# Kernel optimization log

Hardware: AMD Instinct MI355X
Metric: run time of the kernel (lower is better)

The kernel has to match this reference:

```python
import jax, jax.numpy as jnp
import numpy as np

N_NODES = 100000
N_EDGES = 1600000
N_GRAPHS = 512
IN_C, HID_C, OUT_C = 128, 128, 64


def setup_inputs() -> dict:
    key = jax.random.key(0)
    ks = jax.random.split(key, 10)
    x = jax.random.normal(ks[0], (N_NODES, IN_C), dtype=jnp.float32)
    edge_index = jax.random.randint(ks[1], (2, N_EDGES), 0, N_NODES, dtype=jnp.int64)
    batch = jnp.sort(jax.random.randint(ks[2], (N_NODES,), 0, N_GRAPHS, dtype=jnp.int64))
    def glorot(k, shape):
        fan_in = shape[1]
        return jax.random.normal(k, shape, dtype=jnp.float32) / jnp.sqrt(jnp.float32(fan_in))
    return {
        "x": x, "edge_index": edge_index, "batch": batch,
        "w_nbr0": glorot(ks[3], (HID_C, IN_C)), "w_self0": glorot(ks[4], (HID_C, IN_C)), "b0": jnp.zeros((HID_C,), jnp.float32),
        "w_nbr1": glorot(ks[5], (HID_C, HID_C)), "w_self1": glorot(ks[6], (HID_C, HID_C)), "b1": jnp.zeros((HID_C,), jnp.float32),
        "w_nbr2": glorot(ks[7], (OUT_C, HID_C)), "w_self2": glorot(ks[8], (OUT_C, HID_C)), "b2": jnp.zeros((OUT_C,), jnp.float32),
    }


def _sage_conv(x, src, dst, w_nbr, w_self, b):
    n = x.shape[0]
    # mean aggregation of neighbor messages: gather x[src], segment-sum at dst
    agg = jax.ops.segment_sum(x[src], dst, num_segments=n)  # [N, d]
    deg = jax.ops.segment_sum(jnp.ones_like(dst, dtype=x.dtype), dst, num_segments=n)
    mean_nbr = agg / jnp.maximum(deg, 1.0)[:, None]
    return mean_nbr @ w_nbr.T + x @ w_self.T + b


def reference(x, edge_index, batch, w_nbr0, w_self0, b0, w_nbr1, w_self1, b1, w_nbr2, w_self2, b2):
    src, dst = edge_index[0], edge_index[1]
    h = jax.nn.relu(_sage_conv(x, src, dst, w_nbr0, w_self0, b0))
    h = jax.nn.relu(_sage_conv(h, src, dst, w_nbr1, w_self1, b1))
    h = _sage_conv(h, src, dst, w_nbr2, w_self2, b2)
    # global mean pool over graphs in the batch
    sums = jax.ops.segment_sum(h, batch, num_segments=N_GRAPHS)  # [G, out]
    cnts = jax.ops.segment_sum(jnp.ones_like(batch, dtype=h.dtype), batch, num_segments=N_GRAPHS)
    return sums / jnp.maximum(cnts, 1.0)[:, None]
```

## Files before the change

### kernel.cpp

```cpp
#include <hip/hip_runtime.h>
#include <hip/hip_bf16.h>

#define NGRAPHS 512
#define BCAP 8192

typedef __attribute__((ext_vector_type(8))) short bf16x8;
typedef __attribute__((ext_vector_type(4))) float f32x4;

__device__ inline short f2bf(float x) {
    __hip_bfloat16 h = __float2bfloat16(x);
    return *(short*)&h;
}
__device__ inline float bflo(uint v) { return __uint_as_float(v << 16); }
__device__ inline float bfhi(uint v) { return __uint_as_float(v & 0xffff0000u); }


__global__ __launch_bounds__(256) void k_bscatter(const int* __restrict__ src,
                                                  const int* __restrict__ dst,
                                                  int* __restrict__ bcur,
                                                  uint* __restrict__ pairs,
                                                  int nE, int NB) {
    __shared__ int cnt[512];
    __shared__ int gbase[512];
    const int t = threadIdx.x;
    const int seg0 = blockIdx.x * 4096;

    for (int l = t; l < NB; l += 256) cnt[l] = 0;
    __syncthreads();

    int sv[16], bv[16], rv[16];
#pragma unroll
    for (int k = 0; k < 16; ++k) {
        int e = seg0 + k * 256 + t;
        if (e < nE) {
            int d = dst[e];
            bv[k] = d >> 8;
            rv[k] = atomicAdd(&cnt[bv[k]], 1);
            sv[k] = src[e] | ((d & 255) << 20);
        } else {
            bv[k] = -1;
        }
    }
    __syncthreads();
    for (int l = t; l < NB; l += 256) {
        int c = cnt[l];
        gbase[l] = (c > 0) ? atomicAdd(&bcur[l], c) : 0;
    }
    __syncthreads();
#pragma unroll
    for (int k = 0; k < 16; ++k) {
        if (bv[k] >= 0) {
            int pos = gbase[bv[k]] + rv[k];
            if (pos < BCAP) pairs[(size_t)bv[k] * BCAP + pos] = (uint)sv[k];
        }
    }
}

__global__ __launch_bounds__(256) void k_bbuild(const int* __restrict__ bcur,
                                                const uint* __restrict__ pairs,
                                                int* __restrict__ row_start,
                                                int* __restrict__ row_end,
                                                float* __restrict__ rdeg,
                                                int* __restrict__ col, int n) {
    __shared__ int s[256];
    __shared__ int cur[256];
    const int b = blockIdx.x;
    const int t = threadIdx.x;
    const uint* bp = pairs + (size_t)b * BCAP;
    int cnt = bcur[b];
    if (cnt > BCAP) cnt = BCAP;

    s[t] = 0;
    __syncthreads();
    for (int i = t; i < cnt; i += 256) {
        int local = bp[i] >> 20;
        atomicAdd(&s[local], 1);
    }
    __syncthreads();
    int my = s[t];
    for (int off = 1; off < 256; off <<= 1) {
        int v = (t >= off) ? s[t - off] : 0;
        __syncthreads();
        s[t] += v;
        __syncthreads();
    }
    int excl = s[t] - my;
    int v = b * 256 + t;
    if (v < n) {
        row_start[v] = b * BCAP + excl;
        row_end[v] = b * BCAP + excl + my;
        rdeg[v] = 1.0f / (float)(my > 1 ? my : 1);
    }
    cur[t] = excl;
    __syncthreads();
    for (int i = t; i < cnt; i += 256) {
        uint u = bp[i];
        int local = u >> 20;
        int pos = atomicAdd(&cur[local], 1);
        col[(size_t)b * BCAP + pos] = (int)(u & 0xFFFFFu);
    }
}


__global__ __launch_bounds__(256) void k_cast(const float* __restrict__ x,
                                              ushort* __restrict__ xb, int total4) {
    int i = blockIdx.x * 256 + threadIdx.x;
    if (i >= total4) return;
    float4 v = ((const float4*)x)[i];
    ushort4 o;
    o.x = (ushort)f2bf(v.x);
    o.y = (ushort)f2bf(v.y);
    o.z = (ushort)f2bf(v.z);
    o.w = (ushort)f2bf(v.w);
    ((ushort4*)xb)[i] = o;
}


__global__ __launch_bounds__(256) void k_agg(const ushort* __restrict__ h,
                                             const int* __restrict__ row_start,
                                             const int* __restrict__ row_end,
                                             const int* __restrict__ col,
                                             const float* __restrict__ rdeg,
                                             ushort* __restrict__ out, int n) {
    int w = (blockIdx.x * blockDim.x + threadIdx.x) >> 6;
    int lane = threadIdx.x & 63;
    if (w >= n) return;
    int s = row_start[w], e = row_end[w];
    int grp = lane >> 4;
    int cl = lane & 15;

    float a0 = 0.f, a1 = 0.f, a2 = 0.f, a3 = 0.f, a4 = 0.f, a5 = 0.f, a6 = 0.f, a7 = 0.f;

    if (e > s) {
        int cfirst = col[s];
        for (int j = s; j < e; j += 8) {
            int j0 = j + grp, j1 = j + 4 + grp;
            bool ok0 = j0 < e, ok1 = j1 < e;
            int c0 = ok0 ? col[j0] : cfirst;
            int c1 = ok1 ? col[j1] : cfirst;
            uint4 r0 = *(const uint4*)(h + (size_t)c0 * 128 + cl * 8);
            uint4 r1 = *(const uint4*)(h + (size_t)c1 * 128 + cl * 8);
            if (ok0) {
                a0 += bflo(r0.x); a1 += bfhi(r0.x);
                a2 += bflo(r0.y); a3 += bfhi(r0.y);
                a4 += bflo(r0.z); a5 += bfhi(r0.z);
                a6 += bflo(r0.w); a7 += bfhi(r0.w);
            }
            if (ok1) {
                a0 += bflo(r1.x); a1 += bfhi(r1.x);
                a2 += bflo(r1.y); a3 += bfhi(r1.y);
                a4 += bflo(r1.z); a5 += bfhi(r1.z);
                a6 += bflo(r1.w); a7 += bfhi(r1.w);
            }
        }
        a0 += __shfl_xor(a0, 16); a1 += __shfl_xor(a1, 16);
        a2 += __shfl_xor(a2, 16); a3 += __shfl_xor(a3, 16);
        a4 += __shfl_xor(a4, 16); a5 += __shfl_xor(a5, 16);
        a6 += __shfl_xor(a6, 16); a7 += __shfl_xor(a7, 16);
        a0 += __shfl_xor(a0, 32); a1 += __shfl_xor(a1, 32);
        a2 += __shfl_xor(a2, 32); a3 += __shfl_xor(a3, 32);
        a4 += __shfl_xor(a4, 32); a5 += __shfl_xor(a5, 32);
        a6 += __shfl_xor(a6, 32); a7 += __shfl_xor(a7, 32);
    }

    if (grp == 0) {
        float r = rdeg[w];
        uint4 o;
        o.x = (uint)(ushort)f2bf(a0 * r) | ((uint)(ushort)f2bf(a1 * r) << 16);
        o.y = (uint)(ushort)f2bf(a2 * r) | ((uint)(ushort)f2bf(a3 * r) << 16);
        o.z = (uint)(ushort)f2bf(a4 * r) | ((uint)(ushort)f2bf(a5 * r) << 16);
        o.w = (uint)(ushort)f2bf(a6 * r) | ((uint)(ushort)f2bf(a7 * r) << 16);
        *(uint4*)(out + (size_t)w * 128 + cl * 8) = o;
    }
}


__global__ __launch_bounds__(256) void k_agg2(const ushort* __restrict__ t2,
                                              const int* __restrict__ row_start,
                                              const int* __restrict__ row_end,
                                              const int* __restrict__ col,
                                              const float* __restrict__ rdeg,
                                              ushort* __restrict__ out, int n) {
    int w = (blockIdx.x * blockDim.x + threadIdx.x) >> 6;
    int lane = threadIdx.x & 63;
    if (w >= n) return;
    int s = row_start[w], e = row_end[w];
    int grp = lane >> 4;
    int cl = lane & 15;

    float a0 = 0.f, a1 = 0.f, a2 = 0.f, a3 = 0.f;

    if (e > s) {
        int cfirst = col[s];
        for (int j = s; j < e; j += 8) {
            int j0 = j + grp, j1 = j + 4 + grp;
            bool ok0 = j0 < e, ok1 = j1 < e;
            int c0 = ok0 ? col[j0] : cfirst;
            int c1 = ok1 ? col[j1] : cfirst;
            uint2 r0 = *(const uint2*)(t2 + (size_t)c0 * 128 + cl * 4);
            uint2 r1 = *(const uint2*)(t2 + (size_t)c1 * 128 + cl * 4);
            if (ok0) {
                a0 += bflo(r0.x); a1 += bfhi(r0.x);
                a2 += bflo(r0.y); a3 += bfhi(r0.y);
            }
            if (ok1) {
                a0 += bflo(r1.x); a1 += bfhi(r1.x);
                a2 += bflo(r1.y); a3 += bfhi(r1.y);
            }
        }
        a0 += __shfl_xor(a0, 16); a1 += __shfl_xor(a1, 16);
        a2 += __shfl_xor(a2, 16); a3 += __shfl_xor(a3, 16);
        a0 += __shfl_xor(a0, 32); a1 += __shfl_xor(a1, 32);
        a2 += __shfl_xor(a2, 32); a3 += __shfl_xor(a3, 32);
    }

    if (grp == 0) {
        float r = rdeg[w];
        uint2 tsv = *(const uint2*)(t2 + (size_t)w * 128 + 64 + cl * 4);
        float t0 = bflo(tsv.x), t1 = bfhi(tsv.x);
        float t2v = bflo(tsv.y), t3 = bfhi(tsv.y);
        uint2 o;
        o.x = (uint)(ushort)f2bf(a0 * r + t0) | ((uint)(ushort)f2bf(a1 * r + t1) << 16);
        o.y = (uint)(ushort)f2bf(a2 * r + t2v) | ((uint)(ushort)f2bf(a3 * r + t3) << 16);
        *(uint2*)(out + (size_t)w * 64 + cl * 4) = o;
    }
}


__global__ void k_wprep(const float* __restrict__ wn, const float* __restrict__ ws,
                        short* __restrict__ whi, short* __restrict__ wlo, int outc) {
    int i = blockIdx.x * 256 + threadIdx.x;
    if (i >= outc * 256) return;
    int c = i >> 8, k = i & 255;
    float w = (k < 128) ? wn[c * 128 + k] : ws[c * 128 + k - 128];
    short hi = f2bf(w);
    __hip_bfloat16 hb = *(__hip_bfloat16*)&hi;
    float hif = __bfloat162float(hb);
    whi[i] = hi;
    wlo[i] = f2bf(w - hif);
}

__global__ void k_wprep2(const float* __restrict__ wn, const float* __restrict__ ws,
                         short* __restrict__ whi, short* __restrict__ wlo) {
    int i = blockIdx.x * 256 + threadIdx.x;
    if (i >= 128 * 128) return;
    int c = i >> 7, k = i & 127;
    float w = (c < 64) ? wn[c * 128 + k] : ws[(c - 64) * 128 + k];
    short hi = f2bf(w);
    __hip_bfloat16 hb = *(__hip_bfloat16*)&hi;
    float hif = __bfloat162float(hb);
    whi[i] = hi;
    wlo[i] = f2bf(w - hif);
}


template <int KH, bool RELU, bool HALFBIAS, int CHUNK>
__global__ __launch_bounds__(512) void k_transform2(
    const ushort* __restrict__ meanbuf, const ushort* __restrict__ hbuf,
    const bf16x8* __restrict__ whi, const bf16x8* __restrict__ wlo,
    const float* __restrict__ bias, ushort* __restrict__ out, int n, int nTiles) {
    constexpr int ROWB = KH * 256;
    constexpr int KS = KH * 4;
    __shared__ ushort lds[2][16 * KH * 128];

    const int t = threadIdx.x;
    const int wave = t >> 6, lane = t & 63;
    const int lmod = lane & 15, lgrp = lane >> 4;
    const int c = wave * 16 + lmod;

    bf16x8 bh[KS], bl[KS];
#pragma unroll
    for (int ks = 0; ks < KS; ++ks) {
        int idx = c * (KH * 16) + ks * 4 + lgrp;
        bh[ks] = whi[idx];
        bl[ks] = wlo[idx];
    }
    float bv;
    if (HALFBIAS) bv = (c >= 64) ? bias[c - 64] : 0.f;
    else bv = bias[c];

    const int srow = t >> 5;
    const int seg = t & 31;
    const int tile0 = blockIdx.x * CHUNK;
    if (tile0 >= nTiles) return;
    const int nt = (nTiles - tile0 < CHUNK) ? (nTiles - tile0) : CHUNK;
    const int swr = (srow * ROWB + seg * (KH == 2 ? 16 : 8)) ^ ((srow & 7) << 4);

    uint4 R;
    {
        int m = tile0 * 16 + srow; if (m >= n) m = n - 1;
        if constexpr (KH == 2) {
            const ushort* sp = (seg < 16) ? (meanbuf + (size_t)m * 128 + seg * 8)
                                          : (hbuf + (size_t)m * 128 + (seg - 16) * 8);
            R = *(const uint4*)sp;
        } else {
            uint2 r2 = *(const uint2*)(hbuf + (size_t)m * 128 + seg * 4);
            R.x = r2.x; R.y = r2.y;
        }
    }
    if constexpr (KH == 2) *(uint4*)((char*)lds[0] + swr) = R;
    else { uint2 r2; r2.x = R.x; r2.y = R.y; *(uint2*)((char*)lds[0] + swr) = r2; }
    {
        int m = (tile0 + 1) * 16 + srow; if (m >= n) m = n - 1;
        if constexpr (KH == 2) {
            const ushort* sp = (seg < 16) ? (meanbuf + (size_t)m * 128 + seg * 8)
                                          : (hbuf + (size_t)m * 128 + (seg - 16) * 8);
            R = *(const uint4*)sp;
        } else {
            uint2 r2 = *(const uint2*)(hbuf + (size_t)m * 128 + seg * 4);
            R.x = r2.x; R.y = r2.y;
        }
    }

    for (int tt = 0; tt < nt; ++tt) {
        __syncthreads();
        if (tt + 1 < nt) {
            if constexpr (KH == 2) *(uint4*)((char*)lds[(tt + 1) & 1] + swr) = R;
            else { uint2 r2; r2.x = R.x; r2.y = R.y; *(uint2*)((char*)lds[(tt + 1) & 1] + swr) = r2; }
        }
        if (tt + 2 < nt) {
            int m = (tile0 + tt + 2) * 16 + srow; if (m >= n) m = n - 1;
            if constexpr (KH == 2) {
                const ushort* sp = (seg < 16) ? (meanbuf + (size_t)m * 128 + seg * 8)
                                              : (hbuf + (size_t)m * 128 + (seg - 16) * 8);
                R = *(const uint4*)sp;
            } else {
                uint2 r2 = *(const uint2*)(hbuf + (size_t)m * 128 + seg * 4);
                R.x = r2.x; R.y = r2.y;
            }
        }

        bf16x8 af[KS];
#pragma unroll
        for (int ks = 0; ks < KS; ++ks) {
            int byte = (lmod * ROWB + ks * 64 + lgrp * 16) ^ ((lmod & 7) << 4);
            af[ks] = *(const bf16x8*)((const char*)lds[tt & 1] + byte);
        }
        f32x4 ah = {0.f, 0.f, 0.f, 0.f}, al = {0.f, 0.f, 0.f, 0.f};
#pragma unroll
        for (int ks = 0; ks < KS; ++ks) {
            ah = __builtin_amdgcn_mfma_f32_16x16x32_bf16(af[ks], bh[ks], ah, 0, 0, 0);
            al = __builtin_amdgcn_mfma_f32_16x16x32_bf16(af[ks], bl[ks], al, 0, 0, 0);
        }
        int row0 = (tile0 + tt) * 16;
#pragma unroll
        for (int r = 0; r < 4; ++r) {
            int rr = row0 + lgrp * 4 + r;
            float v = ah[r] + al[r] + bv;
            if (RELU) v = fmaxf(v, 0.f);
            if (rr < n) out[(size_t)rr * 128 + c] = (ushort)f2bf(v);
        }
    }
}


__global__ void k_gbounds(const int* __restrict__ batch, int* __restrict__ gstart, int n) {
    int g = blockIdx.x * blockDim.x + threadIdx.x;
    if (g > NGRAPHS) return;
    int lo = 0, hi = n;
    while (lo < hi) {
        int mid = (lo + hi) >> 1;
        if (batch[mid] < g) lo = mid + 1; else hi = mid;
    }
    gstart[g] = lo;
}

__global__ __launch_bounds__(256) void k_pool2(const ushort* __restrict__ h,
                                               const int* __restrict__ gstart,
                                               float* __restrict__ out) {
    int g = blockIdx.x;
    int t = threadIdx.x, lane = t & 63, wv = t >> 6;
    int s = gstart[g], e = gstart[g + 1];
    float acc = 0.f;
    for (int i = s + wv; i < e; i += 4) {
        uint v = h[(size_t)i * 64 + lane];
        acc += __uint_as_float(v << 16);
    }
    __shared__ float red[4][64];
    red[wv][lane] = acc;
    __syncthreads();
    if (wv == 0) {
        float tot = red[0][lane] + red[1][lane] + red[2][lane] + red[3][lane];
        float c = (float)(e - s);
        out[g * 64 + lane] = tot / fmaxf(c, 1.0f);
    }
}


extern "C" void kernel_launch(void* const* d_in, const int* in_sizes, int n_in,
                              void* d_out, int out_size, void* d_ws, size_t ws_size,
                              hipStream_t stream) {
    const float* x = (const float*)d_in[0];
    const int* ei = (const int*)d_in[1];
    const int* batch = (const int*)d_in[2];
    const float* wn0 = (const float*)d_in[3];
    const float* ws0 = (const float*)d_in[4];
    const float* b0 = (const float*)d_in[5];
    const float* wn1 = (const float*)d_in[6];
    const float* ws1 = (const float*)d_in[7];
    const float* b1 = (const float*)d_in[8];
    const float* wn2 = (const float*)d_in[9];
    const float* ws2 = (const float*)d_in[10];
    const float* b2 = (const float*)d_in[11];

    const int n = in_sizes[0] / 128;
    const int nE = in_sizes[1] / 2;
    const int* src = ei;
    const int* dst = ei + nE;
    const int NB = (n + 255) >> 8;

    char* p = (char*)d_ws;
    auto alloc = [&](size_t bytes) {
        void* r = (void*)p;
        p += (bytes + 255) & ~(size_t)255;
        return r;
    };
    int* bcur = (int*)alloc((size_t)NB * 4);
    uint* pairs = (uint*)alloc((size_t)NB * BCAP * 4);
    int* col = (int*)alloc((size_t)NB * BCAP * 4);
    int* row_start = (int*)alloc((size_t)NB * 256 * 4);
    int* row_end = (int*)alloc((size_t)NB * 256 * 4);
    float* rdeg = (float*)alloc((size_t)NB * 256 * 4);
    int* gstart = (int*)alloc((size_t)(NGRAPHS + 1) * 4);
    short* whi0 = (short*)alloc(128 * 256 * 2);
    short* wlo0 = (short*)alloc(128 * 256 * 2);
    short* whi1 = (short*)alloc(128 * 256 * 2);
    short* wlo1 = (short*)alloc(128 * 256 * 2);
    short* whi2 = (short*)alloc(128 * 128 * 2);
    short* wlo2 = (short*)alloc(128 * 128 * 2);
    ushort* xb = (ushort*)alloc((size_t)n * 128 * 2);
    ushort* meanb = (ushort*)alloc((size_t)n * 128 * 2);
    ushort* h1 = (ushort*)alloc((size_t)n * 128 * 2);
    ushort* h2 = (ushort*)alloc((size_t)n * 128 * 2);
    ushort* h3 = (ushort*)alloc((size_t)n * 64 * 2);

    (void)hipMemsetAsync(bcur, 0, (size_t)NB * 4, stream);

    const int tb = 256;

    k_bscatter<<<(nE + 4095) / 4096, tb, 0, stream>>>(src, dst, bcur, pairs, nE, NB);
    k_bbuild<<<NB, tb, 0, stream>>>(bcur, pairs, row_start, row_end, rdeg, col, n);

    k_cast<<<((n * 128 / 4) + 255) / 256, 256, 0, stream>>>(x, xb, n * 128 / 4);

    k_wprep<<<(128 * 256 + 255) / 256, 256, 0, stream>>>(wn0, ws0, whi0, wlo0, 128);
    k_wprep<<<(128 * 256 + 255) / 256, 256, 0, stream>>>(wn1, ws1, whi1, wlo1, 128);
    k_wprep2<<<(128 * 128 + 255) / 256, 256, 0, stream>>>(wn2, ws2, whi2, wlo2);

    k_gbounds<<<3, 256, 0, stream>>>(batch, gstart, n);

    const int aggGrid = ((n * 64) + tb - 1) / tb;
    const int nTiles = (n + 15) / 16;
    const int CH = 13;
    const int tGrid = (nTiles + CH - 1) / CH;

    k_agg<<<aggGrid, tb, 0, stream>>>(xb, row_start, row_end, col, rdeg, meanb, n);
    k_transform2<2, true, false, 13><<<tGrid, 512, 0, stream>>>(
        meanb, xb, (const bf16x8*)whi0, (const bf16x8*)wlo0, b0, h1, n, nTiles);
    k_agg<<<aggGrid, tb, 0, stream>>>(h1, row_start, row_end, col, rdeg, meanb, n);
    k_transform2<2, true, false, 13><<<tGrid, 512, 0, stream>>>(
        meanb, h1, (const bf16x8*)whi1, (const bf16x8*)wlo1, b1, h2, n, nTiles);
    k_transform2<1, false, true, 13><<<tGrid, 512, 0, stream>>>(
        h2, h2, (const bf16x8*)whi2, (const bf16x8*)wlo2, b2, meanb, n, nTiles);
    k_agg2<<<aggGrid, tb, 0, stream>>>(meanb, row_start, row_end, col, rdeg, h3, n);

    k_pool2<<<NGRAPHS, 256, 0, stream>>>(h3, gstart, (float*)d_out);
}
```

Before: 324.8 us.

## Slice node features into 16-channel planes so aggregation gathers stay cache-resident

Stores node features in a sliced layout of eight planes, each holding 16 channels for all nodes. Aggregation runs one block per slice, so each gather pass touches a 3.2 MB working set that can stay in L2 instead of the full feature matrix. The cast, transform store and load paths, and the final aggregation are all changed to read and write this layout. In exchange each gathered row is only 32 bytes, which means more gather instructions and more index loads per edge. The extra blocks also reread the CSR indices once per slice.

```diff
diff --git a/kernel.cpp b/kernel.cpp
--- a/kernel.cpp
+++ b/kernel.cpp
@@ -13,6 +13,7 @@
 }
 __device__ inline float bflo(uint v) { return __uint_as_float(v << 16); }
 __device__ inline float bfhi(uint v) { return __uint_as_float(v & 0xffff0000u); }
+
 
 
 __global__ __launch_bounds__(256) void k_bscatter(const int* __restrict__ src,
@@ -103,126 +104,94 @@
 
 
 __global__ __launch_bounds__(256) void k_cast(const float* __restrict__ x,
-                                              ushort* __restrict__ xb, int total4) {
+                                              ushort* __restrict__ xb, int n) {
     int i = blockIdx.x * 256 + threadIdx.x;
-    if (i >= total4) return;
-    float4 v = ((const float4*)x)[i];
+    if (i >= n * 32) return;
+    int node = i >> 5, chq = i & 31;
+    int s = chq >> 2, c4 = (chq & 3) * 4;
+    float4 v = *(const float4*)(x + (size_t)node * 128 + chq * 4);
     ushort4 o;
     o.x = (ushort)f2bf(v.x);
     o.y = (ushort)f2bf(v.y);
     o.z = (ushort)f2bf(v.z);
     o.w = (ushort)f2bf(v.w);
-    ((ushort4*)xb)[i] = o;
-}
-
-
-__global__ __launch_bounds__(256) void k_agg(const ushort* __restrict__ h,
-                                             const int* __restrict__ row_start,
-                                             const int* __restrict__ row_end,
-                                             const int* __restrict__ col,
-                                             const float* __restrict__ rdeg,
-                                             ushort* __restrict__ out, int n) {
-    int w = (blockIdx.x * blockDim.x + threadIdx.x) >> 6;
-    int lane = threadIdx.x & 63;
-    if (w >= n) return;
-    int s = row_start[w], e = row_end[w];
-    int grp = lane >> 4;
-    int cl = lane & 15;
-
-    float a0 = 0.f, a1 = 0.f, a2 = 0.f, a3 = 0.f, a4 = 0.f, a5 = 0.f, a6 = 0.f, a7 = 0.f;
-
-    if (e > s) {
-        int cfirst = col[s];
-        for (int j = s; j < e; j += 8) {
-            int j0 = j + grp, j1 = j + 4 + grp;
-            bool ok0 = j0 < e, ok1 = j1 < e;
-            int c0 = ok0 ? col[j0] : cfirst;
-            int c1 = ok1 ? col[j1] : cfirst;
-            uint4 r0 = *(const uint4*)(h + (size_t)c0 * 128 + cl * 8);
-            uint4 r1 = *(const uint4*)(h + (size_t)c1 * 128 + cl * 8);
-            if (ok0) {
-                a0 += bflo(r0.x); a1 += bfhi(r0.x);
-                a2 += bflo(r0.y); a3 += bfhi(r0.y);
-                a4 += bflo(r0.z); a5 += bfhi(r0.z);
-                a6 += bflo(r0.w); a7 += bfhi(r0.w);
-            }
-            if (ok1) {
-                a0 += bflo(r1.x); a1 += bfhi(r1.x);
-                a2 += bflo(r1.y); a3 += bfhi(r1.y);
-                a4 += bflo(r1.z); a5 += bfhi(r1.z);
-                a6 += bflo(r1.w); a7 += bfhi(r1.w);
-            }
-        }
-        a0 += __shfl_xor(a0, 16); a1 += __shfl_xor(a1, 16);
-        a2 += __shfl_xor(a2, 16); a3 += __shfl_xor(a3, 16);
-        a4 += __shfl_xor(a4, 16); a5 += __shfl_xor(a5, 16);
-        a6 += __shfl_xor(a6, 16); a7 += __shfl_xor(a7, 16);
-        a0 += __shfl_xor(a0, 32); a1 += __shfl_xor(a1, 32);
-        a2 += __shfl_xor(a2, 32); a3 += __shfl_xor(a3, 32);
-        a4 += __shfl_xor(a4, 32); a5 += __shfl_xor(a5, 32);
-        a6 += __shfl_xor(a6, 32); a7 += __shfl_xor(a7, 32);
-    }
-
-    if (grp == 0) {
-        float r = rdeg[w];
-        uint4 o;
-        o.x = (uint)(ushort)f2bf(a0 * r) | ((uint)(ushort)f2bf(a1 * r) << 16);
-        o.y = (uint)(ushort)f2bf(a2 * r) | ((uint)(ushort)f2bf(a3 * r) << 16);
-        o.z = (uint)(ushort)f2bf(a4 * r) | ((uint)(ushort)f2bf(a5 * r) << 16);
-        o.w = (uint)(ushort)f2bf(a6 * r) | ((uint)(ushort)f2bf(a7 * r) << 16);
-        *(uint4*)(out + (size_t)w * 128 + cl * 8) = o;
-    }
-}
-
-
-__global__ __launch_bounds__(256) void k_agg2(const ushort* __restrict__ t2,
+    *(ushort4*)(xb + ((size_t)s * n + node) * 16 + c4) = o;
+}
+
+
+__global__ __launch_bounds__(256) void k_aggs(const ushort* __restrict__ hs,
                                               const int* __restrict__ row_start,
                                               const int* __restrict__ row_end,
                                               const int* __restrict__ col,
                                               const float* __restrict__ rdeg,
-                                              ushort* __restrict__ out, int n) {
-    int w = (blockIdx.x * blockDim.x + threadIdx.x) >> 6;
+                                              ushort* __restrict__ outs, int n) {
+    int blk = blockIdx.x;
+    int s = blk & 7;
+    int w = (blk >> 3) * 4 + (threadIdx.x >> 6);
+    if (w >= n) return;
     int lane = threadIdx.x & 63;
+    int eg = lane >> 3, chh = lane & 7;
+    int b0 = row_start[w], e = row_end[w];
+    float a0 = 0.f, a1 = 0.f;
+    const ushort* base = hs + (size_t)s * n * 16;
+
+    if (e > b0) {
+        int cfirst = col[b0];
+        for (int j = b0; j < e; j += 8) {
+            int jj = j + eg;
+            bool ok = jj < e;
+            int c = ok ? col[jj] : cfirst;
+            uint v = *(const uint*)(base + (size_t)c * 16 + chh * 2);
+            if (ok) { a0 += bflo(v); a1 += bfhi(v); }
+        }
+        a0 += __shfl_xor(a0, 8);  a1 += __shfl_xor(a1, 8);
+        a0 += __shfl_xor(a0, 16); a1 += __shfl_xor(a1, 16);
+        a0 += __shfl_xor(a0, 32); a1 += __shfl_xor(a1, 32);
+    }
+    if (eg == 0) {
+        float r = rdeg[w];
+        uint o = (uint)(ushort)f2bf(a0 * r) | ((uint)(ushort)f2bf(a1 * r) << 16);
+        *(uint*)(outs + ((size_t)s * n + w) * 16 + chh * 2) = o;
+    }
+}
+
+
+__global__ __launch_bounds__(256) void k_agg2s(const ushort* __restrict__ t2s,
+                                               const int* __restrict__ row_start,
+                                               const int* __restrict__ row_end,
+                                               const int* __restrict__ col,
+                                               const float* __restrict__ rdeg,
+                                               ushort* __restrict__ out, int n) {
+    int blk = blockIdx.x;
+    int s = blk & 3;
+    int w = (blk >> 2) * 4 + (threadIdx.x >> 6);
     if (w >= n) return;
-    int s = row_start[w], e = row_end[w];
-    int grp = lane >> 4;
-    int cl = lane & 15;
-
-    float a0 = 0.f, a1 = 0.f, a2 = 0.f, a3 = 0.f;
-
-    if (e > s) {
-        int cfirst = col[s];
-        for (int j = s; j < e; j += 8) {
-            int j0 = j + grp, j1 = j + 4 + grp;
-            bool ok0 = j0 < e, ok1 = j1 < e;
-            int c0 = ok0 ? col[j0] : cfirst;
-            int c1 = ok1 ? col[j1] : cfirst;
-            uint2 r0 = *(const uint2*)(t2 + (size_t)c0 * 128 + cl * 4);
-            uint2 r1 = *(const uint2*)(t2 + (size_t)c1 * 128 + cl * 4);
-            if (ok0) {
-                a0 += bflo(r0.x); a1 += bfhi(r0.x);
-                a2 += bflo(r0.y); a3 += bfhi(r0.y);
-            }
-            if (ok1) {
-                a0 += bflo(r1.x); a1 += bfhi(r1.x);
-                a2 += bflo(r1.y); a3 += bfhi(r1.y);
-            }
-        }
+    int lane = threadIdx.x & 63;
+    int eg = lane >> 3, chh = lane & 7;
+    int b0 = row_start[w], e = row_end[w];
+    float a0 = 0.f, a1 = 0.f;
+    const ushort* base = t2s + (size_t)s * n * 16;
+
+    if (e > b0) {
+        int cfirst = col[b0];
+        for (int j = b0; j < e; j += 8) {
+            int jj = j + eg;
+            bool ok = jj < e;
+            int c = ok ? col[jj] : cfirst;
+            uint v = *(const uint*)(base + (size_t)c * 16 + chh * 2);
+            if (ok) { a0 += bflo(v); a1 += bfhi(v); }
+        }
+        a0 += __shfl_xor(a0, 8);  a1 += __shfl_xor(a1, 8);
         a0 += __shfl_xor(a0, 16); a1 += __shfl_xor(a1, 16);
-        a2 += __shfl_xor(a2, 16); a3 += __shfl_xor(a3, 16);
         a0 += __shfl_xor(a0, 32); a1 += __shfl_xor(a1, 32);
-        a2 += __shfl_xor(a2, 32); a3 += __shfl_xor(a3, 32);
-    }
-
-    if (grp == 0) {
+    }
+    if (eg == 0) {
         float r = rdeg[w];
-        uint2 tsv = *(const uint2*)(t2 + (size_t)w * 128 + 64 + cl * 4);
-        float t0 = bflo(tsv.x), t1 = bfhi(tsv.x);
-        float t2v = bflo(tsv.y), t3 = bfhi(tsv.y);
-        uint2 o;
-        o.x = (uint)(ushort)f2bf(a0 * r + t0) | ((uint)(ushort)f2bf(a1 * r + t1) << 16);
-        o.y = (uint)(ushort)f2bf(a2 * r + t2v) | ((uint)(ushort)f2bf(a3 * r + t3) << 16);
-        *(uint2*)(out + (size_t)w * 64 + cl * 4) = o;
+        uint tv = *(const uint*)(t2s + ((size_t)(s + 4) * n + w) * 16 + chh * 2);
+        float v0 = a0 * r + bflo(tv);
+        float v1 = a1 * r + bfhi(tv);
+        uint o = (uint)(ushort)f2bf(v0) | ((uint)(ushort)f2bf(v1) << 16);
+        *(uint*)(out + (size_t)w * 64 + s * 16 + chh * 2) = o;
     }
 }
 
@@ -254,6 +223,22 @@
 }
 
 
+template <int KH>
+__device__ inline uint4 loadA(const ushort* __restrict__ meanbuf,
+                              const ushort* __restrict__ hbuf, int n, int m, int seg) {
+    uint4 R;
+    if constexpr (KH == 2) {
+        const ushort* sp = (seg < 16)
+            ? (meanbuf + ((size_t)(seg >> 1) * n + m) * 16 + (seg & 1) * 8)
+            : (hbuf + ((size_t)((seg - 16) >> 1) * n + m) * 16 + ((seg - 16) & 1) * 8);
+        R = *(const uint4*)sp;
+    } else {
+        uint2 r2 = *(const uint2*)(hbuf + ((size_t)(seg >> 2) * n + m) * 16 + (seg & 3) * 4);
+        R.x = r2.x; R.y = r2.y; R.z = 0; R.w = 0;
+    }
+    return R;
+}
+
 template <int KH, bool RELU, bool HALFBIAS, int CHUNK>
 __global__ __launch_bounds__(512) void k_transform2(
     const ushort* __restrict__ meanbuf, const ushort* __restrict__ hbuf,
@@ -289,27 +274,13 @@
     uint4 R;
     {
         int m = tile0 * 16 + srow; if (m >= n) m = n - 1;
-        if constexpr (KH == 2) {
-            const ushort* sp = (seg < 16) ? (meanbuf + (size_t)m * 128 + seg * 8)
-                                          : (hbuf + (size_t)m * 128 + (seg - 16) * 8);
-            R = *(const uint4*)sp;
-        } else {
-            uint2 r2 = *(const uint2*)(hbuf + (size_t)m * 128 + seg * 4);
-            R.x = r2.x; R.y = r2.y;
-        }
+        R = loadA<KH>(meanbuf, hbuf, n, m, seg);
     }
     if constexpr (KH == 2) *(uint4*)((char*)lds[0] + swr) = R;
     else { uint2 r2; r2.x = R.x; r2.y = R.y; *(uint2*)((char*)lds[0] + swr) = r2; }
     {
         int m = (tile0 + 1) * 16 + srow; if (m >= n) m = n - 1;
-        if constexpr (KH == 2) {
-            const ushort* sp = (seg < 16) ? (meanbuf + (size_t)m * 128 + seg * 8)
-                                          : (hbuf + (size_t)m * 128 + (seg - 16) * 8);
-            R = *(const uint4*)sp;
-        } else {
-            uint2 r2 = *(const uint2*)(hbuf + (size_t)m * 128 + seg * 4);
-            R.x = r2.x; R.y = r2.y;
-        }
+        R = loadA<KH>(meanbuf, hbuf, n, m, seg);
     }
 
     for (int tt = 0; tt < nt; ++tt) {
@@ -320,14 +291,7 @@
         }
         if (tt + 2 < nt) {
             int m = (tile0 + tt + 2) * 16 + srow; if (m >= n) m = n - 1;
-            if constexpr (KH == 2) {
-                const ushort* sp = (seg < 16) ? (meanbuf + (size_t)m * 128 + seg * 8)
-                                              : (hbuf + (size_t)m * 128 + (seg - 16) * 8);
-                R = *(const uint4*)sp;
-            } else {
-                uint2 r2 = *(const uint2*)(hbuf + (size_t)m * 128 + seg * 4);
-                R.x = r2.x; R.y = r2.y;
-            }
+            R = loadA<KH>(meanbuf, hbuf, n, m, seg);
         }
 
         bf16x8 af[KS];
@@ -348,7 +312,7 @@
             int rr = row0 + lgrp * 4 + r;
             float v = ah[r] + al[r] + bv;
             if (RELU) v = fmaxf(v, 0.f);
-            if (rr < n) out[(size_t)rr * 128 + c] = (ushort)f2bf(v);
+            if (rr < n) out[((size_t)wave * n + rr) * 16 + lmod] = (ushort)f2bf(v);
         }
     }
 }
@@ -441,7 +405,7 @@
     k_bscatter<<<(nE + 4095) / 4096, tb, 0, stream>>>(src, dst, bcur, pairs, nE, NB);
     k_bbuild<<<NB, tb, 0, stream>>>(bcur, pairs, row_start, row_end, rdeg, col, n);
 
-    k_cast<<<((n * 128 / 4) + 255) / 256, 256, 0, stream>>>(x, xb, n * 128 / 4);
+    k_cast<<<((n * 32) + 255) / 256, 256, 0, stream>>>(x, xb, n);
 
     k_wprep<<<(128 * 256 + 255) / 256, 256, 0, stream>>>(wn0, ws0, whi0, wlo0, 128);
     k_wprep<<<(128 * 256 + 255) / 256, 256, 0, stream>>>(wn1, ws1, whi1, wlo1, 128);
@@ -449,20 +413,22 @@
 
     k_gbounds<<<3, 256, 0, stream>>>(batch, gstart, n);
 
-    const int aggGrid = ((n * 64) + tb - 1) / tb;
+    const int npb4 = (n + 3) / 4;
+    const int aggGrid = 8 * npb4;
+    const int agg2Grid = 4 * npb4;
     const int nTiles = (n + 15) / 16;
     const int CH = 13;
     const int tGrid = (nTiles + CH - 1) / CH;
 
-    k_agg<<<aggGrid, tb, 0, stream>>>(xb, row_start, row_end, col, rdeg, meanb, n);
+    k_aggs<<<aggGrid, tb, 0, stream>>>(xb, row_start, row_end, col, rdeg, meanb, n);
     k_transform2<2, true, false, 13><<<tGrid, 512, 0, stream>>>(
         meanb, xb, (const bf16x8*)whi0, (const bf16x8*)wlo0, b0, h1, n, nTiles);
-    k_agg<<<aggGrid, tb, 0, stream>>>(h1, row_start, row_end, col, rdeg, meanb, n);
+    k_aggs<<<aggGrid, tb, 0, stream>>>(h1, row_start, row_end, col, rdeg, meanb, n);
     k_transform2<2, true, false, 13><<<tGrid, 512, 0, stream>>>(
         meanb, h1, (const bf16x8*)whi1, (const bf16x8*)wlo1, b1, h2, n, nTiles);
     k_transform2<1, false, true, 13><<<tGrid, 512, 0, stream>>>(
         h2, h2, (const bf16x8*)whi2, (const bf16x8*)wlo2, b2, meanb, n, nTiles);
-    k_agg2<<<aggGrid, tb, 0, stream>>>(meanb, row_start, row_end, col, rdeg, h3, n);
+    k_agg2s<<<agg2Grid, tb, 0, stream>>>(meanb, row_start, row_end, col, rdeg, h3, n);
 
     k_pool2<<<NGRAPHS, 256, 0, stream>>>(h3, gstart, (float*)d_out);
 }
```

After: 744.2 us. 2.29x slower.

## Fuse layer-2 and layer-3 transforms and sort CSR neighbor lists

Applied to the files above, without the earlier changes.

Merges the second SAGE layer's transform with the third layer's projection in one kernel, keeping the ReLU'd hidden tile in LDS instead of writing and rereading it from global memory, and drops one launch. Also sorts each row's column indices in LDS during CSR build to improve gather locality in aggregation. Costs extra registers and a second barrier per tile in the fused kernel, plus a serial per-row insertion sort and 32KB of LDS in the build kernel.

```diff
diff --git a/kernel.cpp b/kernel.cpp
--- a/kernel.cpp
+++ b/kernel.cpp
@@ -56,6 +56,7 @@
     }
 }
 
+
 __global__ __launch_bounds__(256) void k_bbuild(const int* __restrict__ bcur,
                                                 const uint* __restrict__ pairs,
                                                 int* __restrict__ row_start,
@@ -64,6 +65,7 @@
                                                 int* __restrict__ col, int n) {
     __shared__ int s[256];
     __shared__ int cur[256];
+    __shared__ int colbuf[BCAP];
     const int b = blockIdx.x;
     const int t = threadIdx.x;
     const uint* bp = pairs + (size_t)b * BCAP;
@@ -97,8 +99,17 @@
         uint u = bp[i];
         int local = u >> 20;
         int pos = atomicAdd(&cur[local], 1);
-        col[(size_t)b * BCAP + pos] = (int)(u & 0xFFFFFu);
-    }
+        colbuf[pos] = (int)(u & 0xFFFFFu);
+    }
+    __syncthreads();
+    for (int a = excl + 1; a < excl + my; ++a) {
+        int key = colbuf[a];
+        int q = a - 1;
+        while (q >= excl && colbuf[q] > key) { colbuf[q + 1] = colbuf[q]; --q; }
+        colbuf[q + 1] = key;
+    }
+    __syncthreads();
+    for (int i = t; i < cnt; i += 256) col[(size_t)b * BCAP + i] = colbuf[i];
 }
 
 
@@ -254,91 +265,69 @@
 }
 
 
-template <int KH, bool RELU, bool HALFBIAS, int CHUNK>
+template <bool RELU, int CHUNK>
 __global__ __launch_bounds__(512) void k_transform2(
     const ushort* __restrict__ meanbuf, const ushort* __restrict__ hbuf,
     const bf16x8* __restrict__ whi, const bf16x8* __restrict__ wlo,
     const float* __restrict__ bias, ushort* __restrict__ out, int n, int nTiles) {
-    constexpr int ROWB = KH * 256;
-    constexpr int KS = KH * 4;
-    __shared__ ushort lds[2][16 * KH * 128];
+    constexpr int ROWB = 512;
+    __shared__ ushort lds[2][16 * 256];
 
     const int t = threadIdx.x;
     const int wave = t >> 6, lane = t & 63;
     const int lmod = lane & 15, lgrp = lane >> 4;
     const int c = wave * 16 + lmod;
 
-    bf16x8 bh[KS], bl[KS];
-#pragma unroll
-    for (int ks = 0; ks < KS; ++ks) {
-        int idx = c * (KH * 16) + ks * 4 + lgrp;
+    bf16x8 bh[8], bl[8];
+#pragma unroll
+    for (int ks = 0; ks < 8; ++ks) {
+        int idx = c * 32 + ks * 4 + lgrp;
         bh[ks] = whi[idx];
         bl[ks] = wlo[idx];
     }
-    float bv;
-    if (HALFBIAS) bv = (c >= 64) ? bias[c - 64] : 0.f;
-    else bv = bias[c];
+    float bv = bias[c];
 
     const int srow = t >> 5;
     const int seg = t & 31;
     const int tile0 = blockIdx.x * CHUNK;
     if (tile0 >= nTiles) return;
     const int nt = (nTiles - tile0 < CHUNK) ? (nTiles - tile0) : CHUNK;
-    const int swr = (srow * ROWB + seg * (KH == 2 ? 16 : 8)) ^ ((srow & 7) << 4);
+    const int swr = (srow * ROWB + seg * 16) ^ ((srow & 7) << 4);
 
     uint4 R;
     {
         int m = tile0 * 16 + srow; if (m >= n) m = n - 1;
-        if constexpr (KH == 2) {
+        const ushort* sp = (seg < 16) ? (meanbuf + (size_t)m * 128 + seg * 8)
+                                      : (hbuf + (size_t)m * 128 + (seg - 16) * 8);
+        R = *(const uint4*)sp;
+    }
+    *(uint4*)((char*)lds[0] + swr) = R;
+    {
+        int m = (tile0 + 1) * 16 + srow; if (m >= n) m = n - 1;
+        const ushort* sp = (seg < 16) ? (meanbuf + (size_t)m * 128 + seg * 8)
+                                      : (hbuf + (size_t)m * 128 + (seg - 16) * 8);
+        R = *(const uint4*)sp;
+    }
+
+    for (int tt = 0; tt < nt; ++tt) {
+        __syncthreads();
+        if (tt + 1 < nt) *(uint4*)((char*)lds[(tt + 1) & 1] + swr) = R;
+        if (tt + 2 < nt) {
+            int m = (tile0 + tt + 2) * 16 + srow; if (m >= n) m = n - 1;
             const ushort* sp = (seg < 16) ? (meanbuf + (size_t)m * 128 + seg * 8)
                                           : (hbuf + (size_t)m * 128 + (seg - 16) * 8);
             R = *(const uint4*)sp;
-        } else {
-            uint2 r2 = *(const uint2*)(hbuf + (size_t)m * 128 + seg * 4);
-            R.x = r2.x; R.y = r2.y;
-        }
-    }
-    if constexpr (KH == 2) *(uint4*)((char*)lds[0] + swr) = R;
-    else { uint2 r2; r2.x = R.x; r2.y = R.y; *(uint2*)((char*)lds[0] + swr) = r2; }
-    {
-        int m = (tile0 + 1) * 16 + srow; if (m >= n) m = n - 1;
-        if constexpr (KH == 2) {
-            const ushort* sp = (seg < 16) ? (meanbuf + (size_t)m * 128 + seg * 8)
-                                          : (hbuf + (size_t)m * 128 + (seg - 16) * 8);
-            R = *(const uint4*)sp;
-        } else {
-            uint2 r2 = *(const uint2*)(hbuf + (size_t)m * 128 + seg * 4);
-            R.x = r2.x; R.y = r2.y;
-        }
-    }
-
-    for (int tt = 0; tt < nt; ++tt) {
-        __syncthreads();
-        if (tt + 1 < nt) {
-            if constexpr (KH == 2) *(uint4*)((char*)lds[(tt + 1) & 1] + swr) = R;
-            else { uint2 r2; r2.x = R.x; r2.y = R.y; *(uint2*)((char*)lds[(tt + 1) & 1] + swr) = r2; }
-        }
-        if (tt + 2 < nt) {
-            int m = (tile0 + tt + 2) * 16 + srow; if (m >= n) m = n - 1;
-            if constexpr (KH == 2) {
-                const ushort* sp = (seg < 16) ? (meanbuf + (size_t)m * 128 + seg * 8)
-                                              : (hbuf + (size_t)m * 128 + (seg - 16) * 8);
-                R = *(const uint4*)sp;
-            } else {
-                uint2 r2 = *(const uint2*)(hbuf + (size_t)m * 128 + seg * 4);
-                R.x = r2.x; R.y = r2.y;
-            }
-        }
-
-        bf16x8 af[KS];
-#pragma unroll
-        for (int ks = 0; ks < KS; ++ks) {
+        }
+
+        bf16x8 af[8];
+#pragma unroll
+        for (int ks = 0; ks < 8; ++ks) {
             int byte = (lmod * ROWB + ks * 64 + lgrp * 16) ^ ((lmod & 7) << 4);
             af[ks] = *(const bf16x8*)((const char*)lds[tt & 1] + byte);
         }
         f32x4 ah = {0.f, 0.f, 0.f, 0.f}, al = {0.f, 0.f, 0.f, 0.f};
 #pragma unroll
-        for (int ks = 0; ks < KS; ++ks) {
+        for (int ks = 0; ks < 8; ++ks) {
             ah = __builtin_amdgcn_mfma_f32_16x16x32_bf16(af[ks], bh[ks], ah, 0, 0, 0);
             al = __builtin_amdgcn_mfma_f32_16x16x32_bf16(af[ks], bl[ks], al, 0, 0, 0);
         }
@@ -348,6 +337,115 @@
             int rr = row0 + lgrp * 4 + r;
             float v = ah[r] + al[r] + bv;
             if (RELU) v = fmaxf(v, 0.f);
+            if (rr < n) out[(size_t)rr * 128 + c] = (ushort)f2bf(v);
+        }
+    }
+}
+
+
+template <int CHUNK>
+__global__ __launch_bounds__(512) void k_transform_fused(
+    const ushort* __restrict__ meanbuf, const ushort* __restrict__ hbuf,
+    const bf16x8* __restrict__ whi1, const bf16x8* __restrict__ wlo1,
+    const float* __restrict__ bias1,
+    const bf16x8* __restrict__ whi2, const bf16x8* __restrict__ wlo2,
+    const float* __restrict__ bias2,
+    ushort* __restrict__ out, int n, int nTiles) {
+    constexpr int ROWB = 512;
+    __shared__ ushort lds[2][16 * 256];
+    __shared__ ushort hlds[16 * 128];
+
+    const int t = threadIdx.x;
+    const int wave = t >> 6, lane = t & 63;
+    const int lmod = lane & 15, lgrp = lane >> 4;
+    const int c = wave * 16 + lmod;
+
+    bf16x8 b1h[8], b1l[8], b2h[4], b2l[4];
+#pragma unroll
+    for (int ks = 0; ks < 8; ++ks) {
+        int idx = c * 32 + ks * 4 + lgrp;
+        b1h[ks] = whi1[idx];
+        b1l[ks] = wlo1[idx];
+    }
+#pragma unroll
+    for (int ks = 0; ks < 4; ++ks) {
+        int idx = c * 16 + ks * 4 + lgrp;
+        b2h[ks] = whi2[idx];
+        b2l[ks] = wlo2[idx];
+    }
+    float bv1 = bias1[c];
+    float bv2 = (c >= 64) ? bias2[c - 64] : 0.f;
+
+    const int srow = t >> 5;
+    const int seg = t & 31;
+    const int tile0 = blockIdx.x * CHUNK;
+    if (tile0 >= nTiles) return;
+    const int nt = (nTiles - tile0 < CHUNK) ? (nTiles - tile0) : CHUNK;
+    const int swr = (srow * ROWB + seg * 16) ^ ((srow & 7) << 4);
+
+    uint4 R;
+    {
+        int m = tile0 * 16 + srow; if (m >= n) m = n - 1;
+        const ushort* sp = (seg < 16) ? (meanbuf + (size_t)m * 128 + seg * 8)
+                                      : (hbuf + (size_t)m * 128 + (seg - 16) * 8);
+        R = *(const uint4*)sp;
+    }
+    *(uint4*)((char*)lds[0] + swr) = R;
+    {
+        int m = (tile0 + 1) * 16 + srow; if (m >= n) m = n - 1;
+        const ushort* sp = (seg < 16) ? (meanbuf + (size_t)m * 128 + seg * 8)
+                                      : (hbuf + (size_t)m * 128 + (seg - 16) * 8);
+        R = *(const uint4*)sp;
+    }
+
+    for (int tt = 0; tt < nt; ++tt) {
+        __syncthreads();
+        if (tt + 1 < nt) *(uint4*)((char*)lds[(tt + 1) & 1] + swr) = R;
+        if (tt + 2 < nt) {
+            int m = (tile0 + tt + 2) * 16 + srow; if (m >= n) m = n - 1;
+            const ushort* sp = (seg < 16) ? (meanbuf + (size_t)m * 128 + seg * 8)
+                                          : (hbuf + (size_t)m * 128 + (seg - 16) * 8);
+            R = *(const uint4*)sp;
+        }
+
+        bf16x8 af[8];
+#pragma unroll
+        for (int ks = 0; ks < 8; ++ks) {
+            int byte = (lmod * ROWB + ks * 64 + lgrp * 16) ^ ((lmod & 7) << 4);
+            af[ks] = *(const bf16x8*)((const char*)lds[tt & 1] + byte);
+        }
+        f32x4 ah = {0.f, 0.f, 0.f, 0.f}, al = {0.f, 0.f, 0.f, 0.f};
+#pragma unroll
+        for (int ks = 0; ks < 8; ++ks) {
+            ah = __builtin_amdgcn_mfma_f32_16x16x32_bf16(af[ks], b1h[ks], ah, 0, 0, 0);
+            al = __builtin_amdgcn_mfma_f32_16x16x32_bf16(af[ks], b1l[ks], al, 0, 0, 0);
+        }
+#pragma unroll
+        for (int r = 0; r < 4; ++r) {
+            int rr16 = lgrp * 4 + r;
+            float v = fmaxf(ah[r] + al[r] + bv1, 0.f);
+            int byte = ((rr16 * 256 + (c >> 3) * 16) ^ ((rr16 & 7) << 4)) + (c & 7) * 2;
+            *(ushort*)((char*)hlds + byte) = (ushort)f2bf(v);
+        }
+        __syncthreads();
+
+        bf16x8 af2[4];
+#pragma unroll
+        for (int ks = 0; ks < 4; ++ks) {
+            int byte = (lmod * 256 + ks * 64 + lgrp * 16) ^ ((lmod & 7) << 4);
+            af2[ks] = *(const bf16x8*)((const char*)hlds + byte);
+        }
+        f32x4 ch = {0.f, 0.f, 0.f, 0.f}, cl2 = {0.f, 0.f, 0.f, 0.f};
+#pragma unroll
+        for (int ks = 0; ks < 4; ++ks) {
+            ch = __builtin_amdgcn_mfma_f32_16x16x32_bf16(af2[ks], b2h[ks], ch, 0, 0, 0);
+            cl2 = __builtin_amdgcn_mfma_f32_16x16x32_bf16(af2[ks], b2l[ks], cl2, 0, 0, 0);
+        }
+        int row0 = (tile0 + tt) * 16;
+#pragma unroll
+        for (int r = 0; r < 4; ++r) {
+            int rr = row0 + lgrp * 4 + r;
+            float v = ch[r] + cl2[r] + bv2;
             if (rr < n) out[(size_t)rr * 128 + c] = (ushort)f2bf(v);
         }
     }
@@ -431,7 +529,7 @@
     ushort* xb = (ushort*)alloc((size_t)n * 128 * 2);
     ushort* meanb = (ushort*)alloc((size_t)n * 128 * 2);
     ushort* h1 = (ushort*)alloc((size_t)n * 128 * 2);
-    ushort* h2 = (ushort*)alloc((size_t)n * 128 * 2);
+    ushort* t2 = (ushort*)alloc((size_t)n * 128 * 2);
     ushort* h3 = (ushort*)alloc((size_t)n * 64 * 2);
 
     (void)hipMemsetAsync(bcur, 0, (size_t)NB * 4, stream);
@@ -455,14 +553,13 @@
     const int tGrid = (nTiles + CH - 1) / CH;
 
     k_agg<<<aggGrid, tb, 0, stream>>>(xb, row_start, row_end, col, rdeg, meanb, n);
-    k_transform2<2, true, false, 13><<<tGrid, 512, 0, stream>>>(
+    k_transform2<true, 13><<<tGrid, 512, 0, stream>>>(
         meanb, xb, (const bf16x8*)whi0, (const bf16x8*)wlo0, b0, h1, n, nTiles);
     k_agg<<<aggGrid, tb, 0, stream>>>(h1, row_start, row_end, col, rdeg, meanb, n);
-    k_transform2<2, true, false, 13><<<tGrid, 512, 0, stream>>>(
-        meanb, h1, (const bf16x8*)whi1, (const bf16x8*)wlo1, b1, h2, n, nTiles);
-    k_transform2<1, false, true, 13><<<tGrid, 512, 0, stream>>>(
-        h2, h2, (const bf16x8*)whi2, (const bf16x8*)wlo2, b2, meanb, n, nTiles);
-    k_agg2<<<aggGrid, tb, 0, stream>>>(meanb, row_start, row_end, col, rdeg, h3, n);
+    k_transform_fused<13><<<tGrid, 512, 0, stream>>>(
+        meanb, h1, (const bf16x8*)whi1, (const bf16x8*)wlo1, b1,
+        (const bf16x8*)whi2, (const bf16x8*)wlo2, b2, t2, n, nTiles);
+    k_agg2<<<aggGrid, tb, 0, stream>>>(t2, row_start, row_end, col, rdeg, h3, n);
 
     k_pool2<<<NGRAPHS, 256, 0, stream>>>(h3, gstart, (float*)d_out);
 }
```

New measurement: 363.4 us. 11.9% more time.
